# Kernel optimization log

Measured on AMD Instinct MI355X. Metric: run time of the kernel, lower is better.

The kernel has to match this reference:

```python
import jax, jax.numpy as jnp
import numpy as np
import math

NUM_Q_HEADS = 32
NUM_KV_HEADS = 8


def setup_inputs() -> dict:
    key = jax.random.key(0)
    k1, k2, k3 = jax.random.split(key, 3)
    B, S, E = 2, 2048, 2048
    kv_E = NUM_KV_HEADS * (E // NUM_Q_HEADS)  # 512
    q = jax.random.normal(k1, (B, S, E), dtype=jnp.float32)
    k = jax.random.normal(k2, (B, S, kv_E), dtype=jnp.float32)
    v = jax.random.normal(k3, (B, S, kv_E), dtype=jnp.float32)
    return {"q": q, "k": k, "v": v}


def reference(q, k, v):
    B, S, E = q.shape
    H, KV = NUM_Q_HEADS, NUM_KV_HEADS
    D = E // H
    G = H // KV  # query heads per kv head
    scale = math.sqrt(D)
    # q heads laid out so group g of kv-head h corresponds to q-head h*G+g,
    # matching torch repeat_interleave semantics.
    qh = q.reshape(B, S, KV, G, D).transpose(0, 2, 3, 1, 4)  # [B,KV,G,S,D]
    kh = k.reshape(B, S, KV, D).transpose(0, 2, 1, 3)        # [B,KV,S,D]
    vh = v.reshape(B, S, KV, D).transpose(0, 2, 1, 3)        # [B,KV,S,D]
    scores = jnp.einsum('bkgsd,bktd->bkgst', qh, kh) / scale  # [B,KV,G,S,S]
    weights = jax.nn.softmax(scores, axis=-1)
    out = jnp.einsum('bkgst,bktd->bkgsd', weights, vh)        # [B,KV,G,S,D]
    # back to [B,S,E] with head order (kv_head, group) == q-head index
    return out.transpose(0, 3, 1, 2, 4).reshape(B, S, E)
```

## Files before the change

kernel.cpp:

```cpp
#include <hip/hip_runtime.h>
#include <hip/hip_bf16.h>


#define S_LEN 2048
#define E_DIM 2048
#define KV_E  512
#define D_HEAD 64
#define BN 64
#define NTILE (S_LEN / BN)

typedef __attribute__((ext_vector_type(8))) short short8;
typedef __attribute__((ext_vector_type(4))) float floatx4;

__device__ __forceinline__ short bf(float x) {
    return __builtin_bit_cast(short, __float2bfloat16(x));
}

__global__ __launch_bounds__(256)
void gqa_prepack_kernel(const float* __restrict__ k, const float* __restrict__ v,
                        short* __restrict__ ws) {
    __shared__ float kf[BN][D_HEAD + 2];
    __shared__ float vf[BN][D_HEAD + 2];
    const int kt = blockIdx.x, kvh = blockIdx.y, b = blockIdx.z;
    const int tid = threadIdx.x;
    short* wt = ws + ((size_t)(b * 8 + kvh) * NTILE + kt) * 8192;
    const float* kb = k + ((size_t)(b * S_LEN + kt * BN)) * KV_E + kvh * D_HEAD;
    const float* vb = v + ((size_t)(b * S_LEN + kt * BN)) * KV_E + kvh * D_HEAD;

    #pragma unroll
    for (int i = tid; i < 1024; i += 256) {
        const int r = i >> 4, c0 = (i & 15) << 2;
        floatx4 k4 = *((const floatx4*)(kb + (size_t)r * KV_E + c0));
        floatx4 v4 = *((const floatx4*)(vb + (size_t)r * KV_E + c0));
        kf[r][c0] = k4[0]; kf[r][c0 + 1] = k4[1]; kf[r][c0 + 2] = k4[2]; kf[r][c0 + 3] = k4[3];
        vf[r][c0] = v4[0]; vf[r][c0 + 1] = v4[1]; vf[r][c0 + 2] = v4[2]; vf[r][c0 + 3] = v4[3];
    }
    __syncthreads();
    #pragma unroll
    for (int c = tid; c < 1024; c += 256) {
        const int fk = c >> 6, l = c & 63;
        const int quad = l >> 4, lc = l & 15;
        const int ks = (fk >> 2) & 1, sub = fk & 3;
        short8 s;
        if (fk < 8) {
            const int row = ((lc >> 2) << 3) + (lc & 3) + ((sub & 1) << 2) + ((sub >> 1) << 5);
            const int c0 = ks * 32 + quad * 8;
            #pragma unroll
            for (int j = 0; j < 8; ++j) s[j] = bf(kf[row][c0 + j]);
        } else {
            const int d = sub * 16 + lc;
            const int k0 = ks * 32 + quad * 8;
            #pragma unroll
            for (int j = 0; j < 8; ++j) s[j] = bf(vf[k0 + j][d]);
        }
        *((short8*)(wt + c * 8)) = s;
    }
}

__global__ __launch_bounds__(256, 2)
void GroupedQueryAttention_36163624632989_kernel(
        const float* __restrict__ q,
        const short* __restrict__ ws,
        float* __restrict__ out, const int B) {
    __shared__ short lds[2 * 8192];

    const int f = blockIdx.x;
    const int chunk = gridDim.x >> 3;
    const int wg = (f & 7) * chunk + (f >> 3);
    const int qt = wg & 15;
    const int t2 = wg >> 4;
    const int b  = t2 % B;
    const int hp = t2 / B;
    const int kvh = hp >> 1;

    const int tid  = threadIdx.x;
    const int w    = tid >> 6;
    const int lane = tid & 63;
    const int quad = lane >> 4;
    const int lc   = lane & 15;

    const int h = (hp << 1) + (w & 1);
    const int rowhalf = w >> 1;

    const float SCL = 1.4426950408889634f / 8.0f;

    const short ONE = (short)0x3F80;
    const short8 ones8 = {ONE, ONE, ONE, ONE, ONE, ONE, ONE, ONE};

    short8 aq[4][2];
    #pragma unroll
    for (int mt = 0; mt < 4; ++mt) {
        const int qrow = qt * 128 + rowhalf * 64 + mt * 16 + lc;
        const float* qp = q + ((size_t)(b * S_LEN + qrow)) * E_DIM + h * D_HEAD;
        #pragma unroll
        for (int ks = 0; ks < 2; ++ks) {
            const float* p = qp + ks * 32 + quad * 8;
            floatx4 qa = *((const floatx4*)p);
            floatx4 qb = *((const floatx4*)(p + 4));
            aq[mt][ks][0] = bf(qa[0] * SCL); aq[mt][ks][1] = bf(qa[1] * SCL);
            aq[mt][ks][2] = bf(qa[2] * SCL); aq[mt][ks][3] = bf(qa[3] * SCL);
            aq[mt][ks][4] = bf(qb[0] * SCL); aq[mt][ks][5] = bf(qb[1] * SCL);
            aq[mt][ks][6] = bf(qb[2] * SCL); aq[mt][ks][7] = bf(qb[3] * SCL);
        }
    }

    floatx4 o_acc[4][4];
    floatx4 accL[4];
    #pragma unroll
    for (int mt = 0; mt < 4; ++mt) {
        accL[mt] = (floatx4){0.f, 0.f, 0.f, 0.f};
        #pragma unroll
        for (int i = 0; i < 4; ++i)
            o_acc[mt][i] = (floatx4){0.f, 0.f, 0.f, 0.f};
    }

    const short* wsT = ws + (size_t)(b * 8 + kvh) * NTILE * 8192;

    auto stage = [&](int buf, int kt) {
        const short* src = wsT + (size_t)kt * 8192 + w * 2048 + (lane << 3);
        short* dst = lds + buf * 8192 + w * 2048;
        #pragma unroll
        for (int i = 0; i < 4; ++i)
            __builtin_amdgcn_global_load_lds(
                (const __attribute__((address_space(1))) void*)(src + i * 512),
                (__attribute__((address_space(3))) void*)(dst + i * 512),
                16, 0, 0);
    };

    stage(0, 0);
    __syncthreads();
    int cur = 0;

    for (int kt = 0; kt < NTILE; ++kt) {
        if (kt + 1 < NTILE) stage(cur ^ 1, kt + 1);

        const short* fb = lds + cur * 8192 + (lane << 3);

        floatx4 accT[4][4];
        #pragma unroll
        for (int mt = 0; mt < 4; ++mt)
            #pragma unroll
            for (int t = 0; t < 4; ++t)
                accT[mt][t] = (floatx4){0.f, 0.f, 0.f, 0.f};
        #pragma unroll
        for (int ks = 0; ks < 2; ++ks) {
            short8 bk4[4];
            #pragma unroll
            for (int t = 0; t < 4; ++t)
                bk4[t] = *((const short8*)(fb + (ks * 4 + t) * 512));
            #pragma unroll
            for (int mt = 0; mt < 4; ++mt)
                #pragma unroll
                for (int t = 0; t < 4; ++t)
                    accT[mt][t] = __builtin_amdgcn_mfma_f32_16x16x32_bf16(
                        bk4[t], aq[mt][ks], accT[mt][t], 0, 0, 0);
        }

        #pragma unroll
        for (int ks = 0; ks < 2; ++ks) {
            short8 bv4[4];
            #pragma unroll
            for (int nt = 0; nt < 4; ++nt)
                bv4[nt] = *((const short8*)(fb + (8 + ks * 4 + nt) * 512));
            #pragma unroll
            for (int mt = 0; mt < 4; ++mt) {
                short8 ap;
                #pragma unroll
                for (int r = 0; r < 4; ++r) {
                    ap[r]     = bf(__builtin_amdgcn_exp2f(accT[mt][2 * ks][r]));
                    ap[4 + r] = bf(__builtin_amdgcn_exp2f(accT[mt][2 * ks + 1][r]));
                }
                #pragma unroll
                for (int nt = 0; nt < 4; ++nt)
                    o_acc[mt][nt] = __builtin_amdgcn_mfma_f32_16x16x32_bf16(
                        ap, bv4[nt], o_acc[mt][nt], 0, 0, 0);
                accL[mt] = __builtin_amdgcn_mfma_f32_16x16x32_bf16(
                    ap, ones8, accL[mt], 0, 0, 0);
            }
        }

        __syncthreads();
        cur ^= 1;
    }

    #pragma unroll
    for (int mt = 0; mt < 4; ++mt) {
        float* op = out + (size_t)b * S_LEN * E_DIM + h * D_HEAD;
        #pragma unroll
        for (int r = 0; r < 4; ++r) {
            const float inv_l = 1.0f / accL[mt][r];
            const int grow = qt * 128 + rowhalf * 64 + mt * 16 + quad * 4 + r;
            #pragma unroll
            for (int nt = 0; nt < 4; ++nt)
                op[(size_t)grow * E_DIM + nt * 16 + lc] = o_acc[mt][nt][r] * inv_l;
        }
    }
}

extern "C" void kernel_launch(void* const* d_in, const int* in_sizes, int n_in,
                              void* d_out, int out_size, void* d_ws, size_t ws_size,
                              hipStream_t stream) {
    const float* q = (const float*)d_in[0];
    const float* k = (const float*)d_in[1];
    const float* v = (const float*)d_in[2];
    float* out = (float*)d_out;
    short* ws = (short*)d_ws;
    const int B = in_sizes[0] / (S_LEN * E_DIM);

    dim3 pgrid(NTILE, 8, B);
    gqa_prepack_kernel<<<pgrid, 256, 0, stream>>>(k, v, ws);

    dim3 grid(B * 256);
    GroupedQueryAttention_36163624632989_kernel<<<grid, 256, 0, stream>>>(q, ws, out, B);
}
```

Before: 152.8 us.

## Stage two K/V tiles per barrier and read K directly in prepack

The attention loop now loads two 64-key tiles per stage into a four-buffer LDS ring and processes both before each barrier, which halves the number of __syncthreads per sequence. The first QK MFMA takes a zero accumulator directly instead of zero-initialising one. Prepack drops the K staging in shared memory and reads K straight from global memory. The cost is double the LDS per block (64 KB), which may cut occupancy at launch bound 2, and prepack K reads become strided.

```diff
diff --git a/kernel.cpp b/kernel.cpp
--- a/kernel.cpp
+++ b/kernel.cpp
@@ -19,7 +19,6 @@
 __global__ __launch_bounds__(256)
 void gqa_prepack_kernel(const float* __restrict__ k, const float* __restrict__ v,
                         short* __restrict__ ws) {
-    __shared__ float kf[BN][D_HEAD + 2];
     __shared__ float vf[BN][D_HEAD + 2];
     const int kt = blockIdx.x, kvh = blockIdx.y, b = blockIdx.z;
     const int tid = threadIdx.x;
@@ -30,10 +29,9 @@
     #pragma unroll
     for (int i = tid; i < 1024; i += 256) {
         const int r = i >> 4, c0 = (i & 15) << 2;
-        floatx4 k4 = *((const floatx4*)(kb + (size_t)r * KV_E + c0));
         floatx4 v4 = *((const floatx4*)(vb + (size_t)r * KV_E + c0));
-        kf[r][c0] = k4[0]; kf[r][c0 + 1] = k4[1]; kf[r][c0 + 2] = k4[2]; kf[r][c0 + 3] = k4[3];
-        vf[r][c0] = v4[0]; vf[r][c0 + 1] = v4[1]; vf[r][c0 + 2] = v4[2]; vf[r][c0 + 3] = v4[3];
+        vf[r][c0] = v4[0]; vf[r][c0 + 1] = v4[1];
+        vf[r][c0 + 2] = v4[2]; vf[r][c0 + 3] = v4[3];
     }
     __syncthreads();
     #pragma unroll
@@ -45,8 +43,11 @@
         if (fk < 8) {
             const int row = ((lc >> 2) << 3) + (lc & 3) + ((sub & 1) << 2) + ((sub >> 1) << 5);
             const int c0 = ks * 32 + quad * 8;
-            #pragma unroll
-            for (int j = 0; j < 8; ++j) s[j] = bf(kf[row][c0 + j]);
+            const float* kp = kb + (size_t)row * KV_E + c0;
+            floatx4 a  = *((const floatx4*)kp);
+            floatx4 b2 = *((const floatx4*)(kp + 4));
+            s[0] = bf(a[0]);  s[1] = bf(a[1]);  s[2] = bf(a[2]);  s[3] = bf(a[3]);
+            s[4] = bf(b2[0]); s[5] = bf(b2[1]); s[6] = bf(b2[2]); s[7] = bf(b2[3]);
         } else {
             const int d = sub * 16 + lc;
             const int k0 = ks * 32 + quad * 8;
@@ -62,7 +63,7 @@
         const float* __restrict__ q,
         const short* __restrict__ ws,
         float* __restrict__ out, const int B) {
-    __shared__ short lds[2 * 8192];
+    __shared__ short lds[4 * 8192];
 
     const int f = blockIdx.x;
     const int chunk = gridDim.x >> 3;
@@ -86,6 +87,7 @@
 
     const short ONE = (short)0x3F80;
     const short8 ones8 = {ONE, ONE, ONE, ONE, ONE, ONE, ONE, ONE};
+    const floatx4 ZERO4 = (floatx4){0.f, 0.f, 0.f, 0.f};
 
     short8 aq[4][2];
     #pragma unroll
@@ -127,35 +129,33 @@
                 16, 0, 0);
     };
 
-    stage(0, 0);
-    __syncthreads();
-    int cur = 0;
-
-    for (int kt = 0; kt < NTILE; ++kt) {
-        if (kt + 1 < NTILE) stage(cur ^ 1, kt + 1);
-
-        const short* fb = lds + cur * 8192 + (lane << 3);
-
+    auto body = [&](const short* fbase) {
+        const short* fb = fbase + (lane << 3);
         floatx4 accT[4][4];
-        #pragma unroll
-        for (int mt = 0; mt < 4; ++mt)
+        {
+            short8 bk4[4];
             #pragma unroll
             for (int t = 0; t < 4; ++t)
-                accT[mt][t] = (floatx4){0.f, 0.f, 0.f, 0.f};
-        #pragma unroll
-        for (int ks = 0; ks < 2; ++ks) {
-            short8 bk4[4];
-            #pragma unroll
-            for (int t = 0; t < 4; ++t)
-                bk4[t] = *((const short8*)(fb + (ks * 4 + t) * 512));
+                bk4[t] = *((const short8*)(fb + t * 512));
             #pragma unroll
             for (int mt = 0; mt < 4; ++mt)
                 #pragma unroll
                 for (int t = 0; t < 4; ++t)
                     accT[mt][t] = __builtin_amdgcn_mfma_f32_16x16x32_bf16(
-                        bk4[t], aq[mt][ks], accT[mt][t], 0, 0, 0);
-        }
-
+                        bk4[t], aq[mt][0], ZERO4, 0, 0, 0);
+        }
+        {
+            short8 bk4[4];
+            #pragma unroll
+            for (int t = 0; t < 4; ++t)
+                bk4[t] = *((const short8*)(fb + (4 + t) * 512));
+            #pragma unroll
+            for (int mt = 0; mt < 4; ++mt)
+                #pragma unroll
+                for (int t = 0; t < 4; ++t)
+                    accT[mt][t] = __builtin_amdgcn_mfma_f32_16x16x32_bf16(
+                        bk4[t], aq[mt][1], accT[mt][t], 0, 0, 0);
+        }
         #pragma unroll
         for (int ks = 0; ks < 2; ++ks) {
             short8 bv4[4];
@@ -178,9 +178,20 @@
                     ap, ones8, accL[mt], 0, 0, 0);
             }
         }
-
+    };
+
+    stage(0, 0); stage(1, 1);
+    __syncthreads();
+
+    for (int i = 0; i < NTILE / 2; ++i) {
+        const int base = (i & 1) << 1;
+        if (i + 1 < NTILE / 2) {
+            stage(base ^ 2, 2 * i + 2);
+            stage((base ^ 2) + 1, 2 * i + 3);
+        }
+        body(lds + base * 8192);
+        body(lds + (base + 1) * 8192);
         __syncthreads();
-        cur ^= 1;
     }
 
     #pragma unroll
```

New measurement: 153.3 us. About the same (+0.3%).
